# Performance work log

Measured on AMD Instinct MI355X. Metric: run time of the kernel, lower is better.

The kernel has to match this reference:

```python
import jax, jax.numpy as jnp
import numpy as np

N_PTS = 8_388_608
WIDTH, HEIGHT = 1232.0, 1616.0
K3 = jnp.array([[758.03967, 0.0, 621.46572],
                [0.0, 761.62359, 756.86402],
                [0.0, 0.0, 1.0]], dtype=jnp.float32)
MIN_D_R, MAX_D_R = 1.0, 10.0   # rewards_from_pose defaults
MIN_D_M, MAX_D_M = 1.0, 5.0    # Model pc_clip_limits
DELTA = 0.05
EPS = 1e-6


def euler_xyz(roll, pitch, yaw):
    # pytorch3d euler_angles_to_matrix(angles, 'XYZ') = Rx(roll) @ Ry(pitch) @ Rz(yaw)
    cr, sr = jnp.cos(roll), jnp.sin(roll)
    cp, sp = jnp.cos(pitch), jnp.sin(pitch)
    cy, sy = jnp.cos(yaw), jnp.sin(yaw)
    one, zero = jnp.ones_like(cr), jnp.zeros_like(cr)
    Rx = jnp.array([[one, zero, zero], [zero, cr, -sr], [zero, sr, cr]])
    Ry = jnp.array([[cp, zero, sp], [zero, one, zero], [-sp, zero, cp]])
    Rz = jnp.array([[cy, -sy, zero], [sy, cy, zero], [zero, zero, one]])
    return Rx @ Ry @ Rz


def reward_from_pose(pose, verts):
    # pose: [6] = (x, y, z, roll, pitch, yaw); verts: [N,3]
    x, y, z, roll, pitch, yaw = pose[0], pose[1], pose[2], pose[3], pose[4], pose[5]
    R = euler_xyz(roll, pitch, yaw)                 # [3,3]
    t = jnp.stack([x, y, z])                        # [3]
    v = (verts - t) @ R                             # R_inv @ p == p @ R (R orthonormal); [N,3]
    dist_mask = (v[:, 2] > MIN_D_R) & (v[:, 2] < MAX_D_R)
    p = v @ K3.T                                    # homogeneous image coords [N,3]
    u = p[:, 0] / p[:, 2]
    w = p[:, 1] / p[:, 2]
    fov_mask = (p[:, 2] > 0) & (u > 1) & (u < WIDTH - 1) & (w > 1) & (w < HEIGHT - 1)
    return jnp.sum(dist_mask & fov_mask).astype(jnp.float32)


def setup_inputs() -> dict:
    key = jax.random.key(0)
    points = 5.0 * jax.random.normal(key, (N_PTS, 3), dtype=jnp.float32)
    z0 = jnp.float32(0.0)
    return {"points": points, "x": z0, "y": z0, "z": z0,
            "roll": z0, "pitch": z0, "yaw": z0}


def reference(points, x, y, z, roll, pitch, yaw):
    pose0 = jnp.stack([x, y, z, roll, pitch, yaw])
    # 7 poses: baseline + 6 finite-difference perturbations (as in FrustumVisibilityEst.forward)
    poses = jnp.concatenate([pose0[None], pose0[None] + DELTA * jnp.eye(6, dtype=pose0.dtype)], axis=0)
    rewards = jax.vmap(reward_from_pose, in_axes=(0, None))(poses, points)  # [7]
    reward = rewards[0]
    loss = 1.0 / (reward + EPS)

    # Model.forward geometry path (uses pc_clip_limits = [1, 5])
    R = euler_xyz(roll, pitch, yaw)
    t = jnp.stack([x, y, z])
    vc = (points - t) @ R                           # camera-frame verts [N,3]
    dist_mask = (vc[:, 2] > MIN_D_M) & (vc[:, 2] < MAX_D_M)
    p = vc @ K3.T
    u = p[:, 0] / p[:, 2]
    w = p[:, 1] / p[:, 2]
    fov_mask = (p[:, 2] > 0) & (u > 1) & (u < WIDTH - 1) & (w > 1) & (w < HEIGHT - 1)
    mask = dist_mask & fov_mask
    # original does verts[mask]; we zero out masked-off rows to keep static shapes
    verts_out = jnp.where(mask[:, None], vc, jnp.zeros((), vc.dtype))
    return verts_out, loss
```

## Files before the change

### kernel.cpp

```cpp
#include <hip/hip_runtime.h>

#define N_PTS 8388608
#define FX 758.03967f
#define CXC 621.46572f
#define FY 761.62359f
#define CYC 756.86402f
#define U_MAX 1231.0f
#define W_MAX 1615.0f
#define MIN_D 1.0f
#define MAX_D_R 10.0f
#define MAX_D_M 5.0f

#define PTS_PER_THREAD 8
#define THREADS 256
#define N_THREADS_TOT (N_PTS / PTS_PER_THREAD)
#define N_BLOCKS (N_THREADS_TOT / THREADS)
#define N_WAVES (N_THREADS_TOT / 64)

typedef float vfloat4 __attribute__((ext_vector_type(4)));


__global__ void pose_setup_kernel(const float* __restrict__ x, const float* __restrict__ y,
                                  const float* __restrict__ z, const float* __restrict__ roll,
                                  const float* __restrict__ pitch, const float* __restrict__ yaw,
                                  float* __restrict__ ws) {
    float cr = cosf(*roll), sr = sinf(*roll);
    float cp = cosf(*pitch), sp = sinf(*pitch);
    float cy = cosf(*yaw),  sy = sinf(*yaw);
    ws[0] = cp * cy;                ws[1] = -(cp * sy);             ws[2] = sp;
    ws[3] = cr * sy + sr * sp * cy; ws[4] = cr * cy - sr * sp * sy; ws[5] = -(sr * cp);
    ws[6] = sr * sy - cr * sp * cy; ws[7] = sr * cy + cr * sp * sy; ws[8] = cr * cp;
    ws[9] = *x; ws[10] = *y; ws[11] = *z;
}

__global__ __launch_bounds__(256) void frustum_kernel(const vfloat4* __restrict__ pts,
                                                      const float* __restrict__ ws,
                                                      vfloat4* __restrict__ out,
                                                      unsigned int* __restrict__ parts) {
    const float R0 = ws[0], R1 = ws[1], R2 = ws[2];
    const float R3 = ws[3], R4 = ws[4], R5 = ws[5];
    const float R6 = ws[6], R7 = ws[7], R8 = ws[8];
    const float t0 = ws[9], t1 = ws[10], t2 = ws[11];

    const int tid = blockIdx.x * THREADS + threadIdx.x;
    const long base = (long)tid * 6;

    union Pack { vfloat4 v[6]; float f[24]; };
    Pack in, o;
#pragma unroll
    for (int i = 0; i < 6; ++i) in.v[i] = pts[base + i];

    int cnt = 0;
#pragma unroll
    for (int p = 0; p < PTS_PER_THREAD; ++p) {
        float d0 = in.f[p * 3 + 0] - t0;
        float d1 = in.f[p * 3 + 1] - t1;
        float d2 = in.f[p * 3 + 2] - t2;
        float v0 = fmaf(d2, R6, fmaf(d1, R3, d0 * R0));
        float v1 = fmaf(d2, R7, fmaf(d1, R4, d0 * R1));
        float v2 = fmaf(d2, R8, fmaf(d1, R5, d0 * R2));
        float p0 = fmaf(v2, CXC, v0 * FX);
        float p1 = fmaf(v2, CYC, v1 * FY);
        float u = p0 / v2;
        float w = p1 / v2;
        bool fov = (v2 > 0.0f) && (u > 1.0f) && (u < U_MAX) && (w > 1.0f) && (w < W_MAX);
        bool rew = fov && (v2 > MIN_D) && (v2 < MAX_D_R);
        cnt += (int)__popcll(__ballot(rew));
        bool m = fov && (v2 > MIN_D) && (v2 < MAX_D_M);
        o.f[p * 3 + 0] = m ? v0 : 0.0f;
        o.f[p * 3 + 1] = m ? v1 : 0.0f;
        o.f[p * 3 + 2] = m ? v2 : 0.0f;
    }

#pragma unroll
    for (int i = 0; i < 6; ++i)
        out[base + i] = o.v[i];

    if ((threadIdx.x & 63) == 0)
        parts[tid >> 6] = (unsigned int)cnt;
}

__global__ __launch_bounds__(256) void finalize_kernel(const unsigned int* __restrict__ parts,
                                                       float* __restrict__ out) {
    unsigned int s = 0;
    for (int i = threadIdx.x; i < N_WAVES; i += THREADS) s += parts[i];
    for (int off = 32; off > 0; off >>= 1) s += __shfl_down(s, off, 64);
    __shared__ unsigned int red[4];
    if ((threadIdx.x & 63) == 0) red[threadIdx.x >> 6] = s;
    __syncthreads();
    if (threadIdx.x == 0) {
        unsigned int c = red[0] + red[1] + red[2] + red[3];
        out[(long)3 * N_PTS] = 1.0f / ((float)c + 1e-6f);
    }
}

extern "C" void kernel_launch(void* const* d_in, const int* in_sizes, int n_in,
                              void* d_out, int out_size, void* d_ws, size_t ws_size,
                              hipStream_t stream) {
    const float* points = (const float*)d_in[0];
    const float* x      = (const float*)d_in[1];
    const float* y      = (const float*)d_in[2];
    const float* z      = (const float*)d_in[3];
    const float* roll   = (const float*)d_in[4];
    const float* pitch  = (const float*)d_in[5];
    const float* yaw    = (const float*)d_in[6];
    float* ws = (float*)d_ws;
    unsigned int* parts = (unsigned int*)ws + 16;
    float* out = (float*)d_out;

    pose_setup_kernel<<<1, 1, 0, stream>>>(x, y, z, roll, pitch, yaw, ws);
    frustum_kernel<<<N_BLOCKS, THREADS, 0, stream>>>((const vfloat4*)points, ws,
                                                     (vfloat4*)out, parts);
    finalize_kernel<<<1, THREADS, 0, stream>>>(parts, out);
}
```

Measured before the change: 207.1 us.

## Use grid-stride coalesced float4 streaming with cross-lane shuffles to reassemble xyz points

Replaces the per-thread 6-float4 strided load and store with a grid-stride loop in which each thread loads one consecutive float4 per iteration, so wave accesses are fully contiguous. The xyz triplets that straddle float4 boundaries are rebuilt from neighbouring lanes with shuffles, plus extra scalar loads at wave edges. Each thread transforms two candidate points and counts them so that every point is counted exactly once. In exchange it does redundant transform work (about two transforms per four floats), adds shuffles, phase selects and a modulo, and uses a fixed 2048-block grid.

```diff
diff --git a/kernel.cpp b/kernel.cpp
--- a/kernel.cpp
+++ b/kernel.cpp
@@ -1,6 +1,7 @@
 #include <hip/hip_runtime.h>
 
 #define N_PTS 8388608
+#define N_F4 (N_PTS * 3 / 4)
 #define FX 758.03967f
 #define CXC 621.46572f
 #define FY 761.62359f
@@ -11,11 +12,11 @@
 #define MAX_D_R 10.0f
 #define MAX_D_M 5.0f
 
-#define PTS_PER_THREAD 8
 #define THREADS 256
-#define N_THREADS_TOT (N_PTS / PTS_PER_THREAD)
-#define N_BLOCKS (N_THREADS_TOT / THREADS)
-#define N_WAVES (N_THREADS_TOT / 64)
+#define GRID_BLOCKS 2048
+#define TOTAL_THREADS (GRID_BLOCKS * THREADS)
+#define ITERS (N_F4 / TOTAL_THREADS)
+#define N_WAVES_G (GRID_BLOCKS * (THREADS / 64))
 
 typedef float vfloat4 __attribute__((ext_vector_type(4)));
 
@@ -33,57 +34,80 @@
     ws[9] = *x; ws[10] = *y; ws[11] = *z;
 }
 
-__global__ __launch_bounds__(256) void frustum_kernel(const vfloat4* __restrict__ pts,
-                                                      const float* __restrict__ ws,
-                                                      vfloat4* __restrict__ out,
-                                                      unsigned int* __restrict__ parts) {
+__global__ __launch_bounds__(256) void stream_kernel(const float* __restrict__ ptsf,
+                                                     const float* __restrict__ ws,
+                                                     vfloat4* __restrict__ out4,
+                                                     unsigned int* __restrict__ parts) {
     const float R0 = ws[0], R1 = ws[1], R2 = ws[2];
     const float R3 = ws[3], R4 = ws[4], R5 = ws[5];
     const float R6 = ws[6], R7 = ws[7], R8 = ws[8];
     const float t0 = ws[9], t1 = ws[10], t2 = ws[11];
+    const vfloat4* pts4 = (const vfloat4*)ptsf;
 
-    const int tid = blockIdx.x * THREADS + threadIdx.x;
-    const long base = (long)tid * 6;
+    const int lane = threadIdx.x & 63;
+    int cnt = 0;
 
-    union Pack { vfloat4 v[6]; float f[24]; };
-    Pack in, o;
-#pragma unroll
-    for (int i = 0; i < 6; ++i) in.v[i] = pts[base + i];
-
-    int cnt = 0;
-#pragma unroll
-    for (int p = 0; p < PTS_PER_THREAD; ++p) {
-        float d0 = in.f[p * 3 + 0] - t0;
-        float d1 = in.f[p * 3 + 1] - t1;
-        float d2 = in.f[p * 3 + 2] - t2;
-        float v0 = fmaf(d2, R6, fmaf(d1, R3, d0 * R0));
-        float v1 = fmaf(d2, R7, fmaf(d1, R4, d0 * R1));
-        float v2 = fmaf(d2, R8, fmaf(d1, R5, d0 * R2));
+    auto xform = [&](float px, float py, float pz, float& v0, float& v1, float& v2,
+                     bool& rew, bool& vis) {
+        float d0 = px - t0, d1 = py - t1, d2 = pz - t2;
+        v0 = fmaf(d2, R6, fmaf(d1, R3, d0 * R0));
+        v1 = fmaf(d2, R7, fmaf(d1, R4, d0 * R1));
+        v2 = fmaf(d2, R8, fmaf(d1, R5, d0 * R2));
         float p0 = fmaf(v2, CXC, v0 * FX);
         float p1 = fmaf(v2, CYC, v1 * FY);
         float u = p0 / v2;
         float w = p1 / v2;
         bool fov = (v2 > 0.0f) && (u > 1.0f) && (u < U_MAX) && (w > 1.0f) && (w < W_MAX);
-        bool rew = fov && (v2 > MIN_D) && (v2 < MAX_D_R);
-        cnt += (int)__popcll(__ballot(rew));
-        bool m = fov && (v2 > MIN_D) && (v2 < MAX_D_M);
-        o.f[p * 3 + 0] = m ? v0 : 0.0f;
-        o.f[p * 3 + 1] = m ? v1 : 0.0f;
-        o.f[p * 3 + 2] = m ? v2 : 0.0f;
+        rew = fov && (v2 > MIN_D) && (v2 < MAX_D_R);
+        vis = fov && (v2 > MIN_D) && (v2 < MAX_D_M);
+    };
+
+    for (int it = 0; it < ITERS; ++it) {
+        const int gid = it * TOTAL_THREADS + blockIdx.x * THREADS + threadIdx.x;
+        vfloat4 m = pts4[gid];
+        const int phase = gid % 3;
+        const int g0 = gid * 4;
+
+        float p1f = __shfl_up(m.w, 1, 64);
+        float p2f = __shfl_up(m.z, 1, 64);
+        float n1f = __shfl_down(m.x, 1, 64);
+        float n2f = __shfl_down(m.y, 1, 64);
+        if (lane == 0 && phase != 0) { p2f = ptsf[g0 - 2]; p1f = ptsf[g0 - 1]; }
+        if (lane == 63 && phase != 2) { n1f = ptsf[g0 + 4]; n2f = ptsf[g0 + 5]; }
+
+        float ax = phase == 0 ? m.x : (phase == 1 ? p1f : p2f);
+        float ay = phase == 0 ? m.y : (phase == 1 ? m.x : p1f);
+        float az = phase == 0 ? m.z : (phase == 1 ? m.y : m.x);
+        float bx = phase == 0 ? m.w : (phase == 1 ? m.z : m.y);
+        float by = phase == 0 ? n1f : (phase == 1 ? m.w : m.z);
+        float bz = phase == 0 ? n2f : (phase == 1 ? n1f : m.w);
+
+        float A0, A1, A2, B0, B1, B2;
+        bool rA, vA, rB, vB;
+        xform(ax, ay, az, A0, A1, A2, rA, vA);
+        xform(bx, by, bz, B0, B1, B2, rB, vB);
+        A0 = vA ? A0 : 0.0f; A1 = vA ? A1 : 0.0f; A2 = vA ? A2 : 0.0f;
+        B0 = vB ? B0 : 0.0f; B1 = vB ? B1 : 0.0f; B2 = vB ? B2 : 0.0f;
+
+        cnt += (int)__popcll(__ballot(rA && phase == 0));
+        cnt += (int)__popcll(__ballot(rB));
+
+        vfloat4 o;
+        o.x = phase == 0 ? A0 : (phase == 1 ? A1 : A2);
+        o.y = phase == 0 ? A1 : (phase == 1 ? A2 : B0);
+        o.z = phase == 0 ? A2 : (phase == 1 ? B0 : B1);
+        o.w = phase == 0 ? B0 : (phase == 1 ? B1 : B2);
+        out4[gid] = o;
     }
 
-#pragma unroll
-    for (int i = 0; i < 6; ++i)
-        out[base + i] = o.v[i];
-
-    if ((threadIdx.x & 63) == 0)
-        parts[tid >> 6] = (unsigned int)cnt;
+    if (lane == 0)
+        parts[(blockIdx.x << 2) + (threadIdx.x >> 6)] = (unsigned int)cnt;
 }
 
 __global__ __launch_bounds__(256) void finalize_kernel(const unsigned int* __restrict__ parts,
                                                        float* __restrict__ out) {
     unsigned int s = 0;
-    for (int i = threadIdx.x; i < N_WAVES; i += THREADS) s += parts[i];
+    for (int i = threadIdx.x; i < N_WAVES_G; i += THREADS) s += parts[i];
     for (int off = 32; off > 0; off >>= 1) s += __shfl_down(s, off, 64);
     __shared__ unsigned int red[4];
     if ((threadIdx.x & 63) == 0) red[threadIdx.x >> 6] = s;
@@ -109,7 +133,6 @@
     float* out = (float*)d_out;
 
     pose_setup_kernel<<<1, 1, 0, stream>>>(x, y, z, roll, pitch, yaw, ws);
-    frustum_kernel<<<N_BLOCKS, THREADS, 0, stream>>>((const vfloat4*)points, ws,
-                                                     (vfloat4*)out, parts);
+    stream_kernel<<<GRID_BLOCKS, THREADS, 0, stream>>>(points, ws, (vfloat4*)out, parts);
     finalize_kernel<<<1, THREADS, 0, stream>>>(parts, out);
 }
```

Result: faster. 197.9 us (-4.4%).
